# Optimization experiments

Measured on AMD Instinct MI355X. Metric: run time of the kernel, lower is better.

The kernel has to match this reference:

```python
import jax, jax.numpy as jnp
import numpy as np

N_Q = 50000
B, T = 256, 500
DK = 128      # q_embed_dim == memory_key_state_dim == final_fc_dim
DV = 256      # qa_embed_dim == memory_value_state_dim
M = 50        # memory_size

def setup_inputs() -> dict:
    key = jax.random.key(0)
    ks = jax.random.split(key, 12)
    q_data = jax.random.randint(ks[0], (B, T), 0, N_Q + 1)
    qa_data = jax.random.randint(ks[1], (B, T), 0, 2 * N_Q + 1)
    # target in {-1, 0, 1}; -1 = padding (masked out)
    u = jax.random.uniform(ks[2], (B * T, 1))
    target = jnp.floor(u * 3.0) - 1.0
    # embedding tables with padding_idx=0 zeroed
    q_tab = (jax.random.normal(ks[3], (N_Q + 1, DK)) * (2.0 / DK) ** 0.5).at[0].set(0.0)
    qa_tab = (jax.random.normal(ks[4], (2 * N_Q + 1, DV)) * (2.0 / DV) ** 0.5).at[0].set(0.0)
    Mk = jax.random.normal(ks[5], (M, DK)) * (2.0 / DK) ** 0.5
    Mv0 = jax.random.normal(ks[6], (M, DV)) * (2.0 / DV) ** 0.5
    We = jax.random.normal(ks[7], (DV, DV)) * (1.0 / DV) ** 0.5
    be = jnp.zeros((DV,))
    Wa = jax.random.normal(ks[8], (DV, DV)) * (1.0 / DV) ** 0.5
    ba = jnp.zeros((DV,))
    Wr = jax.random.normal(ks[9], (DK, DV + DK)) * (2.0 / (DV + DK)) ** 0.5
    br = jnp.zeros((DK,))
    Wp = jax.random.normal(ks[10], (1, DK)) * (2.0 / DK) ** 0.5
    bp = jnp.zeros((1,))
    return dict(q_data=q_data, qa_data=qa_data, target=target, q_tab=q_tab,
                qa_tab=qa_tab, Mk=Mk, Mv0=Mv0, We=We, be=be, Wa=Wa, ba=ba,
                Wr=Wr, br=br, Wp=Wp, bp=bp)


def reference(q_data, qa_data, target, q_tab, qa_tab, Mk, Mv0, We, be, Wa, ba, Wr, br, Wp, bp):
    b, t = q_data.shape
    q_e = q_tab[q_data]            # (B,T,DK)
    qa_e = qa_tab[qa_data]         # (B,T,DV)
    wr_mask = (q_data >= 1).astype(q_e.dtype)  # write gate per step
    Mv_init = jnp.broadcast_to(Mv0[None], (b, M, DV))

    def step(Mv, xs):
        q, qa, m = xs              # q:(B,DK) qa:(B,DV) m:(B,)
        w = jax.nn.softmax(q @ Mk.T, axis=-1)          # (B,M) correlation weight
        read = jnp.einsum('bm,bmd->bd', w, Mv)         # (B,DV)
        e = jax.nn.sigmoid(qa @ We.T + be)             # erase (B,DV)
        a = jnp.tanh(qa @ Wa.T + ba)                   # add   (B,DV)
        new = Mv * (1.0 - w[:, :, None] * e[:, None, :]) + w[:, :, None] * a[:, None, :]
        Mv = jnp.where(m[:, None, None] > 0, new, Mv)  # only write for non-pad steps
        return Mv, read

    _, reads = jax.lax.scan(step, Mv_init,
                            (q_e.transpose(1, 0, 2), qa_e.transpose(1, 0, 2), wr_mask.T))
    reads = reads.transpose(1, 0, 2)                    # (B,T,DV)
    feat = jnp.concatenate([reads, q_e], axis=2).reshape(b * t, DV + DK)
    h = jnp.tanh(feat @ Wr.T + br)                      # (B*T,DK)
    pred = h @ Wp.T + bp                                # (B*T,1) logits
    mask = target >= 0
    # stable BCE-with-logits per element
    per = jnp.maximum(pred, 0.0) - pred * target + jnp.log1p(jnp.exp(-jnp.abs(pred)))
    n_valid = jnp.maximum(jnp.sum(mask.astype(pred.dtype)), 1.0)
    loss = jnp.sum(jnp.where(mask, per, 0.0)) / n_valid
    probs = jax.nn.sigmoid(pred)
    return loss, probs
```

## Files before the change

kernel.cpp:

```cpp
#include <hip/hip_runtime.h>
#include <hip/hip_bf16.h>
#include <stdint.h>


#define BATCH 256
#define TLEN  500
#define DKQ   128
#define DVV   256
#define MSZ   50
#define NROWS 128000
#define GSZ   10

__device__ __forceinline__ float bfs(uint16_t u){
  union { uint32_t u; float f; } v; v.u = ((uint32_t)u) << 16; return v.f;
}
__device__ __forceinline__ uint16_t f2b(float x){
  union { __hip_bfloat16 h; uint16_t u; } c; c.h = __float2bfloat16(x); return c.u;
}

typedef __attribute__((ext_vector_type(8))) short bf16x8;
typedef __attribute__((ext_vector_type(4))) float f32x4;

__device__ __forceinline__ void gl_lds16(const void* g, void* l){
  __builtin_amdgcn_global_load_lds(
      (const __attribute__((address_space(1))) void*)g,
      (__attribute__((address_space(3))) void*)l, 16, 0, 0);
}

__global__ __launch_bounds__(128, 1) void k_w(
    const int* __restrict__ q_data, const float* __restrict__ q_tab,
    const float* __restrict__ Mk, float* __restrict__ w_ws)
{
  __shared__ float mk[MSZ*DKQ];
  __shared__ float wt[128*52];
  const int tid = threadIdx.x;
  for (int li = tid; li < 1600; li += 128)
    ((float4*)mk)[li] = ((const float4*)Mk)[li];
  __syncthreads();

  const int row = blockIdx.x*128 + tid;
  const int qi = q_data[row];
  const float4* qrow = (const float4*)(q_tab + (size_t)qi*DKQ);

  float acc[MSZ];
  #pragma unroll
  for (int m=0;m<MSZ;m++) acc[m] = 0.f;

  #pragma unroll 1
  for (int c8=0; c8<8; c8++){
    float4 q0 = qrow[c8*4+0], q1 = qrow[c8*4+1], q2 = qrow[c8*4+2], q3 = qrow[c8*4+3];
    #pragma unroll
    for (int m=0;m<MSZ;m++){
      const float4* mr = (const float4*)&mk[m*DKQ + c8*16];
      float4 a = mr[0], b = mr[1], cc = mr[2], d = mr[3];
      float s = acc[m];
      s = fmaf(q0.x,a.x,s);  s = fmaf(q0.y,a.y,s);  s = fmaf(q0.z,a.z,s);  s = fmaf(q0.w,a.w,s);
      s = fmaf(q1.x,b.x,s);  s = fmaf(q1.y,b.y,s);  s = fmaf(q1.z,b.z,s);  s = fmaf(q1.w,b.w,s);
      s = fmaf(q2.x,cc.x,s); s = fmaf(q2.y,cc.y,s); s = fmaf(q2.z,cc.z,s); s = fmaf(q2.w,cc.w,s);
      s = fmaf(q3.x,d.x,s);  s = fmaf(q3.y,d.y,s);  s = fmaf(q3.z,d.z,s);  s = fmaf(q3.w,d.w,s);
      acc[m] = s;
    }
  }
  float mx = acc[0];
  #pragma unroll
  for (int m=1;m<MSZ;m++) mx = fmaxf(mx, acc[m]);
  float s = 0.f;
  #pragma unroll
  for (int m=0;m<MSZ;m++){ acc[m] = __expf(acc[m]-mx); s += acc[m]; }
  float inv = 1.0f / s;
  #pragma unroll
  for (int m=0;m<MSZ;m++) wt[tid*52+m] = acc[m]*inv;
  wt[tid*52+50] = 0.f; wt[tid*52+51] = 0.f;
  __syncthreads();
  float4* dst = (float4*)(w_ws + (size_t)blockIdx.x*128*52);
  const float4* src = (const float4*)wt;
  for (int li = tid; li < 1664; li += 128) dst[li] = src[li];
}

__global__ __launch_bounds__(256) void k_cvt(
    const float* __restrict__ qa_tab, const float* __restrict__ We,
    const float* __restrict__ Wa, uint16_t* __restrict__ qa_bf,
    uint16_t* __restrict__ wcomb)
{
  const size_t n_qa4 = 6400064;
  const size_t n_w4  = 32768;
  size_t stride = (size_t)gridDim.x*blockDim.x;
  for (size_t i = (size_t)blockIdx.x*256 + threadIdx.x; i < n_qa4 + n_w4; i += stride){
    float4 v;
    if (i < n_qa4){
      v = ((const float4*)qa_tab)[i];
      ushort4 o; o.x=f2b(v.x); o.y=f2b(v.y); o.z=f2b(v.z); o.w=f2b(v.w);
      ((ushort4*)qa_bf)[i] = o;
    } else {
      size_t j = i - n_qa4;
      size_t f = j*4;
      int col = (int)(f >> 8), k = (int)(f & 255);
      const float* srcp = (col < 256) ? (We + (size_t)col*256 + k)
                                      : (Wa + (size_t)(col-256)*256 + k);
      v = *(const float4*)srcp;
      ushort4 o; o.x=f2b(v.x); o.y=f2b(v.y); o.z=f2b(v.z); o.w=f2b(v.w);
      ((ushort4*)wcomb)[j] = o;
    }
  }
}

__global__ __launch_bounds__(256) void k_cvt2(
    const float* __restrict__ q_tab, const float* __restrict__ Wr,
    uint16_t* __restrict__ q_bf, uint16_t* __restrict__ wr_bf)
{
  const size_t n_q4  = 1600032;
  const size_t n_wr4 = 12288;
  size_t stride = (size_t)gridDim.x*blockDim.x;
  for (size_t i = (size_t)blockIdx.x*256 + threadIdx.x; i < n_q4 + n_wr4; i += stride){
    if (i < n_q4){
      float4 v = ((const float4*)q_tab)[i];
      ushort4 o; o.x=f2b(v.x); o.y=f2b(v.y); o.z=f2b(v.z); o.w=f2b(v.w);
      ((ushort4*)q_bf)[i] = o;
    } else {
      size_t j = i - n_q4;
      float4 v = ((const float4*)Wr)[j];
      ushort4 o; o.x=f2b(v.x); o.y=f2b(v.y); o.z=f2b(v.z); o.w=f2b(v.w);
      ((ushort4*)wr_bf)[j] = o;
    }
  }
}

__global__ __launch_bounds__(256, 2) void k_ea(
    const int* __restrict__ qa_data, const uint16_t* __restrict__ qa_bf,
    const uint16_t* __restrict__ wcomb, const float* __restrict__ be,
    const float* __restrict__ ba, __hip_bfloat16* __restrict__ ea_ws)
{
  __shared__ uint16_t Ab[128*32];
  __shared__ uint16_t Bb[128*32];
  const int tid = threadIdx.x;
  const int lane = tid & 63, wid = tid >> 6;
  const int braw = blockIdx.x;
  const int nb = (braw >> 3) & 3;
  const int mb = (braw & 7) | ((braw >> 5) << 3);
  const int rb = mb*128, cb = nb*128;

  const char* qac = (const char*)qa_bf;
  size_t aoff0, aoff1;
  {
    int r0 = wid*32 + (lane>>2);
    aoff0 = (size_t)qa_data[rb + r0]*512      + (size_t)(lane&3)*16;
    aoff1 = (size_t)qa_data[rb + r0 + 16]*512 + (size_t)(lane&3)*16;
  }
  const char* wcb = (const char*)wcomb;
  size_t boff0 = (size_t)(cb + wid*32 + (lane>>2))*512 + (size_t)(lane&3)*16;
  size_t boff1 = boff0 + 16*512;

  const int wr = (wid>>1)*64, wc = (wid&1)*64;
  float bias[4];
  #pragma unroll
  for (int tj=0;tj<4;tj++){
    int colg = cb + wc + tj*16 + (lane&15);
    bias[tj] = (nb<2) ? be[colg] : ba[colg-256];
  }

  f32x4 acc[4][4];
  #pragma unroll
  for (int i=0;i<4;i++){
    #pragma unroll
    for (int j=0;j<4;j++) acc[i][j] = (f32x4)(0.f);
  }

  #pragma unroll 1
  for (int kc=0; kc<8; kc++){
    __syncthreads();
    gl_lds16(qac + aoff0 + (size_t)kc*64, &Ab[(wid*2+0)*512]);
    gl_lds16(qac + aoff1 + (size_t)kc*64, &Ab[(wid*2+1)*512]);
    gl_lds16(wcb + boff0 + (size_t)kc*64, &Bb[(wid*2+0)*512]);
    gl_lds16(wcb + boff1 + (size_t)kc*64, &Bb[(wid*2+1)*512]);
    __syncthreads();
    bf16x8 af[4], bfr[4];
    #pragma unroll
    for (int ti=0;ti<4;ti++)
      af[ti] = *(const bf16x8*)&Ab[(wr + ti*16 + (lane&15))*32 + (lane>>4)*8];
    #pragma unroll
    for (int tj=0;tj<4;tj++)
      bfr[tj] = *(const bf16x8*)&Bb[(wc + tj*16 + (lane&15))*32 + (lane>>4)*8];
    #pragma unroll
    for (int ti=0;ti<4;ti++){
      #pragma unroll
      for (int tj=0;tj<4;tj++)
        acc[ti][tj] = __builtin_amdgcn_mfma_f32_16x16x32_bf16(af[ti], bfr[tj], acc[ti][tj], 0, 0, 0);
    }
  }
  const int rq = (lane>>4)*4, cl = lane&15;
  #pragma unroll
  for (int ti=0;ti<4;ti++){
    #pragma unroll
    for (int r=0;r<4;r++){
      int row = rb + wr + ti*16 + rq + r;
      __hip_bfloat16* orow = ea_ws + (size_t)row*512 + cb + wc;
      #pragma unroll
      for (int tj=0;tj<4;tj++){
        float x = acc[ti][tj][r] + bias[tj];
        float v = (nb<2) ? (1.f/(1.f+__expf(-x)))
                         : (1.f - 2.f/(__expf(2.f*x)+1.f));
        orow[tj*16 + cl] = __float2bfloat16(v);
      }
    }
  }
}

__global__ __launch_bounds__(512, 1) void k_scan(
    const int* __restrict__ q_data, const float* __restrict__ w_ws,
    const uint16_t* __restrict__ ea_ws, const float* __restrict__ Mv0,
    __hip_bfloat16* __restrict__ reads_ws)
{
  __shared__ float wbuf[2][GSZ*52];
  __shared__ float part[2][256];
  const int tid = threadIdx.x;
  const int d = tid & 255, h = tid >> 8;
  const int base = blockIdx.x*TLEN;

  float Mv[28];
  #pragma unroll
  for (int qq=0; qq<7; qq++){
    #pragma unroll
    for (int e=0;e<4;e++){
      int quad = 2*qq + h, m = quad*4 + e;
      Mv[qq*4+e] = (quad <= 12 && m < MSZ) ? Mv0[m*256 + d] : 0.f;
    }
  }

  float4 wreg;
  uint16_t ecur[GSZ], acur[GSZ], enxt[GSZ], anxt[GSZ];
  int qcur[GSZ], qnxt[GSZ];

  if (tid < 130) wreg = ((const float4*)(w_ws + (size_t)base*52))[tid];
  #pragma unroll
  for (int j=0;j<GSZ;j++){
    ecur[j] = ea_ws[(size_t)(base+j)*512 + d];
    acur[j] = ea_ws[(size_t)(base+j)*512 + 256 + d];
    qcur[j] = q_data[base+j];
  }
  if (tid < 130) ((float4*)wbuf[0])[tid] = wreg;
  __syncthreads();

  #pragma unroll 1
  for (int g=0; g<50; g++){
    if (g < 49){
      const int sn = base + (g+1)*GSZ;
      if (tid < 130) wreg = ((const float4*)(w_ws + (size_t)sn*52))[tid];
      #pragma unroll
      for (int j=0;j<GSZ;j++){
        enxt[j] = ea_ws[(size_t)(sn+j)*512 + d];
        anxt[j] = ea_ws[(size_t)(sn+j)*512 + 256 + d];
        qnxt[j] = q_data[sn+j];
      }
    }
    const float* wb = wbuf[g&1];
    const int s0 = base + g*GSZ;
    #pragma unroll
    for (int j=0;j<GSZ;j++){
      const float4* wq = (const float4*)(wb + j*52);
      float ef = bfs(ecur[j]), af = bfs(acur[j]);
      float4 wv[7];
      #pragma unroll
      for (int qq=0; qq<6; qq++) wv[qq] = wq[2*qq + h];
      if (h == 0) wv[6] = wq[12];
      float r0=0.f, r1=0.f, r2=0.f, r3=0.f;
      #pragma unroll
      for (int qq=0; qq<6; qq++){
        r0 = fmaf(wv[qq].x, Mv[qq*4+0], r0);
        r1 = fmaf(wv[qq].y, Mv[qq*4+1], r1);
        r2 = fmaf(wv[qq].z, Mv[qq*4+2], r2);
        r3 = fmaf(wv[qq].w, Mv[qq*4+3], r3);
      }
      if (h == 0){
        r0 = fmaf(wv[6].x, Mv[24], r0);
        r1 = fmaf(wv[6].y, Mv[25], r1);
        r2 = fmaf(wv[6].z, Mv[26], r2);
        r3 = fmaf(wv[6].w, Mv[27], r3);
      }
      float rp = (r0+r1)+(r2+r3);
      if (h == 0) part[j&1][d] = rp;
      __syncthreads();
      if (h == 1){
        float rd = rp + part[j&1][d];
        reads_ws[(size_t)(s0+j)*256 + d] = __float2bfloat16(rd);
      }
      if (qcur[j] > 0){
        #pragma unroll
        for (int qq=0; qq<6; qq++){
          { float tt = fmaf(ef, Mv[qq*4+0], -af); Mv[qq*4+0] = fmaf(-wv[qq].x, tt, Mv[qq*4+0]); }
          { float tt = fmaf(ef, Mv[qq*4+1], -af); Mv[qq*4+1] = fmaf(-wv[qq].y, tt, Mv[qq*4+1]); }
          { float tt = fmaf(ef, Mv[qq*4+2], -af); Mv[qq*4+2] = fmaf(-wv[qq].z, tt, Mv[qq*4+2]); }
          { float tt = fmaf(ef, Mv[qq*4+3], -af); Mv[qq*4+3] = fmaf(-wv[qq].w, tt, Mv[qq*4+3]); }
        }
        if (h == 0){
          { float tt = fmaf(ef, Mv[24], -af); Mv[24] = fmaf(-wv[6].x, tt, Mv[24]); }
          { float tt = fmaf(ef, Mv[25], -af); Mv[25] = fmaf(-wv[6].y, tt, Mv[25]); }
        }
      }
    }
    if (g < 49){
      if (tid < 130) ((float4*)wbuf[(g+1)&1])[tid] = wreg;
      #pragma unroll
      for (int j=0;j<GSZ;j++){ ecur[j]=enxt[j]; acur[j]=anxt[j]; qcur[j]=qnxt[j]; }
    }
    __syncthreads();
  }
}

__global__ __launch_bounds__(256, 2) void k_final(
    const int* __restrict__ q_data, const uint16_t* __restrict__ q_bf,
    const uint16_t* __restrict__ reads16, const uint16_t* __restrict__ wr_bf,
    const float* __restrict__ br, const float* __restrict__ Wp,
    const float* __restrict__ bp, const float* __restrict__ target,
    float* __restrict__ out, float* __restrict__ parts)
{
  __shared__ uint16_t Ab[64*32];
  __shared__ uint16_t Bb[128*32];
  __shared__ float redbuf[8];
  const int tid = threadIdx.x;
  const int lane = tid & 63, wid = tid >> 6;
  const int rb = blockIdx.x * 64;

  const char* rdc = (const char*)reads16;
  const char* qbc = (const char*)q_bf;
  const char* wrc = (const char*)wr_bf;
  const int arow = wid*16 + (lane>>2);
  size_t aoff_r = (size_t)(rb+arow)*512 + (size_t)(lane&3)*16;
  size_t aoff_q = (size_t)q_data[rb+arow]*256 + (size_t)(lane&3)*16;
  size_t boff0  = (size_t)(wid*32 + (lane>>2))*768 + (size_t)(lane&3)*16;
  size_t boff1  = boff0 + 16*768;

  f32x4 acc[8];
  #pragma unroll
  for (int tj=0;tj<8;tj++) acc[tj] = (f32x4)(0.f);

  #pragma unroll 1
  for (int kc=0; kc<12; kc++){
    __syncthreads();
    if (kc < 8) gl_lds16(rdc + aoff_r + (size_t)kc*64,     &Ab[wid*512]);
    else        gl_lds16(qbc + aoff_q + (size_t)(kc-8)*64, &Ab[wid*512]);
    gl_lds16(wrc + boff0 + (size_t)kc*64, &Bb[(wid*2+0)*512]);
    gl_lds16(wrc + boff1 + (size_t)kc*64, &Bb[(wid*2+1)*512]);
    __syncthreads();
    bf16x8 af = *(const bf16x8*)&Ab[(wid*16 + (lane&15))*32 + (lane>>4)*8];
    #pragma unroll
    for (int tj=0;tj<8;tj++){
      bf16x8 bf = *(const bf16x8*)&Bb[(tj*16 + (lane&15))*32 + (lane>>4)*8];
      acc[tj] = __builtin_amdgcn_mfma_f32_16x16x32_bf16(af, bf, acc[tj], 0, 0, 0);
    }
  }
  const int cl = lane & 15, rq = lane >> 4;
  float p[4] = {0.f,0.f,0.f,0.f};
  #pragma unroll
  for (int tj=0;tj<8;tj++){
    int cg = tj*16 + cl;
    float brv = br[cg], wpv = Wp[cg];
    #pragma unroll
    for (int r=0;r<4;r++){
      float x = acc[tj][r] + brv;
      float hh = 1.f - 2.f/(__expf(2.f*x)+1.f);
      p[r] = fmaf(hh, wpv, p[r]);
    }
  }
  #pragma unroll
  for (int off=1; off<16; off<<=1){
    #pragma unroll
    for (int r=0;r<4;r++) p[r] += __shfl_xor(p[r], off);
  }
  float bpv = bp[0];
  float lsum = 0.f, csum = 0.f;
  if (cl == 0){
    #pragma unroll
    for (int r=0;r<4;r++){
      int row = rb + wid*16 + rq*4 + r;
      float pred = p[r] + bpv;
      out[1 + row] = 1.f/(1.f + __expf(-pred));
      float tg = target[row];
      if (tg >= 0.f){
        lsum += fmaxf(pred, 0.f) - pred*tg + log1pf(__expf(-fabsf(pred)));
        csum += 1.f;
      }
    }
  }
  #pragma unroll
  for (int off=16; off<64; off<<=1){
    lsum += __shfl_xor(lsum, off);
    csum += __shfl_xor(csum, off);
  }
  if (lane == 0){ redbuf[wid*2] = lsum; redbuf[wid*2+1] = csum; }
  __syncthreads();
  if (tid == 0){
    parts[blockIdx.x]        = redbuf[0]+redbuf[2]+redbuf[4]+redbuf[6];
    parts[2000 + blockIdx.x] = redbuf[1]+redbuf[3]+redbuf[5]+redbuf[7];
  }
}

__global__ __launch_bounds__(256) void k_loss(
    const float* __restrict__ parts, float* __restrict__ out)
{
  __shared__ float red[8];
  const int tid = threadIdx.x;
  float l = 0.f, cn = 0.f;
  for (int i = tid; i < 2000; i += 256){ l += parts[i]; cn += parts[2000+i]; }
  #pragma unroll
  for (int off=32; off>0; off>>=1){ l += __shfl_xor(l, off); cn += __shfl_xor(cn, off); }
  if ((tid & 63) == 0){ red[(tid>>6)*2] = l; red[(tid>>6)*2+1] = cn; }
  __syncthreads();
  if (tid == 0){
    float L = red[0]+red[2]+red[4]+red[6];
    float C = red[1]+red[3]+red[5]+red[7];
    out[0] = L / fmaxf(C, 1.f);
  }
}

extern "C" void kernel_launch(void* const* d_in, const int* in_sizes, int n_in,
                              void* d_out, int out_size, void* d_ws, size_t ws_size,
                              hipStream_t stream) {
  const int*   q_data  = (const int*)d_in[0];
  const int*   qa_data = (const int*)d_in[1];
  const float* target  = (const float*)d_in[2];
  const float* q_tab   = (const float*)d_in[3];
  const float* qa_tab  = (const float*)d_in[4];
  const float* Mk  = (const float*)d_in[5];
  const float* Mv0 = (const float*)d_in[6];
  const float* We  = (const float*)d_in[7];
  const float* be  = (const float*)d_in[8];
  const float* Wa  = (const float*)d_in[9];
  const float* ba  = (const float*)d_in[10];
  const float* Wr  = (const float*)d_in[11];
  const float* br  = (const float*)d_in[12];
  const float* Wp  = (const float*)d_in[13];
  const float* bp  = (const float*)d_in[14];

  char* ws = (char*)d_ws;
  float*          w_ws     = (float*)ws;
  __hip_bfloat16* ea_ws    = (__hip_bfloat16*)(ws + 26624000);
  uint16_t*       qa_bf    = (uint16_t*)(ws + 157696000);
  uint16_t*       wcomb    = (uint16_t*)(ws + 208896512);
  __hip_bfloat16* reads_ws = (__hip_bfloat16*)(ws + 157696000);
  float*          parts    = (float*)ws;
  uint16_t*       q_bf     = (uint16_t*)(ws + 2000000);
  uint16_t*       wr_bf    = (uint16_t*)(ws + 16000000);

  float* out = (float*)d_out;

  k_w    <<<1000, 128, 0, stream>>>(q_data, q_tab, Mk, w_ws);
  k_cvt  <<<2048, 256, 0, stream>>>(qa_tab, We, Wa, qa_bf, wcomb);
  k_ea   <<<4000, 256, 0, stream>>>(qa_data, qa_bf, wcomb, be, ba, ea_ws);
  k_scan <<<256,  512, 0, stream>>>(q_data, w_ws, (const uint16_t*)ea_ws, Mv0, reads_ws);
  k_cvt2 <<<1024, 256, 0, stream>>>(q_tab, Wr, q_bf, wr_bf);
  k_final<<<2000, 256, 0, stream>>>(q_data, q_bf, (const uint16_t*)reads_ws, wr_bf, br, Wp, bp, target, out, parts);
  k_loss <<<1,    256, 0, stream>>>(parts, out);
}
```

Baseline: 653.0 us.

## Interleave erase/add outputs, pair scan threads via shuffle, enlarge final GEMM tile

k_ea now writes erase and add values interleaved per column, so k_scan fetches both with a single 32-bit load. k_scan maps the two memory halves to adjacent lanes and combines partial reads with a lane shuffle, which removes the per-step __syncthreads and LDS exchange. It also replaces the h==0 branches with a mask multiply and raises launch bounds to 2 blocks per SM. k_final processes 128 rows per block with two A tiles to get more reuse of the B tile, halving the grid and the partial-sum count.

```diff
diff --git a/kernel.cpp b/kernel.cpp
--- a/kernel.cpp
+++ b/kernel.cpp
@@ -13,6 +13,12 @@
 
 __device__ __forceinline__ float bfs(uint16_t u){
   union { uint32_t u; float f; } v; v.u = ((uint32_t)u) << 16; return v.f;
+}
+__device__ __forceinline__ float bflo32(uint32_t u){
+  union { uint32_t u; float f; } v; v.u = u << 16; return v.f;
+}
+__device__ __forceinline__ float bfhi32(uint32_t u){
+  union { uint32_t u; float f; } v; v.u = u & 0xffff0000u; return v.f;
 }
 __device__ __forceinline__ uint16_t f2b(float x){
   union { __hip_bfloat16 h; uint16_t u; } c; c.h = __float2bfloat16(x); return c.u;
@@ -128,7 +134,7 @@
 __global__ __launch_bounds__(256, 2) void k_ea(
     const int* __restrict__ qa_data, const uint16_t* __restrict__ qa_bf,
     const uint16_t* __restrict__ wcomb, const float* __restrict__ be,
-    const float* __restrict__ ba, __hip_bfloat16* __restrict__ ea_ws)
+    const float* __restrict__ ba, uint16_t* __restrict__ ea16)
 {
   __shared__ uint16_t Ab[128*32];
   __shared__ uint16_t Bb[128*32];
@@ -188,53 +194,55 @@
     }
   }
   const int rq = (lane>>4)*4, cl = lane&15;
+  const int isa = (nb >= 2);
+  const int cbase = (cb & 255) + wc;
   #pragma unroll
   for (int ti=0;ti<4;ti++){
     #pragma unroll
     for (int r=0;r<4;r++){
       int row = rb + wr + ti*16 + rq + r;
-      __hip_bfloat16* orow = ea_ws + (size_t)row*512 + cb + wc;
+      uint16_t* orow = ea16 + (size_t)row*512;
       #pragma unroll
       for (int tj=0;tj<4;tj++){
         float x = acc[ti][tj][r] + bias[tj];
         float v = (nb<2) ? (1.f/(1.f+__expf(-x)))
                          : (1.f - 2.f/(__expf(2.f*x)+1.f));
-        orow[tj*16 + cl] = __float2bfloat16(v);
-      }
-    }
-  }
-}
-
-__global__ __launch_bounds__(512, 1) void k_scan(
+        orow[2*(cbase + tj*16 + cl) + isa] = f2b(v);
+      }
+    }
+  }
+}
+
+__global__ __launch_bounds__(512, 2) void k_scan(
     const int* __restrict__ q_data, const float* __restrict__ w_ws,
-    const uint16_t* __restrict__ ea_ws, const float* __restrict__ Mv0,
+    const uint32_t* __restrict__ ea32, const float* __restrict__ Mv0,
     __hip_bfloat16* __restrict__ reads_ws)
 {
   __shared__ float wbuf[2][GSZ*52];
-  __shared__ float part[2][256];
   const int tid = threadIdx.x;
-  const int d = tid & 255, h = tid >> 8;
+  const int d = tid >> 1, h = tid & 1;
   const int base = blockIdx.x*TLEN;
+  const float hm = (h == 0) ? 1.f : 0.f;
 
   float Mv[28];
   #pragma unroll
   for (int qq=0; qq<7; qq++){
+    int quad = 2*qq + h;
     #pragma unroll
     for (int e=0;e<4;e++){
-      int quad = 2*qq + h, m = quad*4 + e;
-      Mv[qq*4+e] = (quad <= 12 && m < MSZ) ? Mv0[m*256 + d] : 0.f;
+      int m = quad*4 + e;
+      Mv[qq*4+e] = (m < MSZ) ? Mv0[m*256 + d] : 0.f;
     }
   }
 
   float4 wreg;
-  uint16_t ecur[GSZ], acur[GSZ], enxt[GSZ], anxt[GSZ];
+  uint32_t eacur[GSZ], eanxt[GSZ];
   int qcur[GSZ], qnxt[GSZ];
 
   if (tid < 130) wreg = ((const float4*)(w_ws + (size_t)base*52))[tid];
   #pragma unroll
   for (int j=0;j<GSZ;j++){
-    ecur[j] = ea_ws[(size_t)(base+j)*512 + d];
-    acur[j] = ea_ws[(size_t)(base+j)*512 + 256 + d];
+    eacur[j] = ea32[(size_t)(base+j)*256 + d];
     qcur[j] = q_data[base+j];
   }
   if (tid < 130) ((float4*)wbuf[0])[tid] = wreg;
@@ -247,8 +255,7 @@
       if (tid < 130) wreg = ((const float4*)(w_ws + (size_t)sn*52))[tid];
       #pragma unroll
       for (int j=0;j<GSZ;j++){
-        enxt[j] = ea_ws[(size_t)(sn+j)*512 + d];
-        anxt[j] = ea_ws[(size_t)(sn+j)*512 + 256 + d];
+        eanxt[j] = ea32[(size_t)(sn+j)*256 + d];
         qnxt[j] = q_data[sn+j];
       }
     }
@@ -257,50 +264,36 @@
     #pragma unroll
     for (int j=0;j<GSZ;j++){
       const float4* wq = (const float4*)(wb + j*52);
-      float ef = bfs(ecur[j]), af = bfs(acur[j]);
+      float ef = bflo32(eacur[j]), af = bfhi32(eacur[j]);
       float4 wv[7];
       #pragma unroll
       for (int qq=0; qq<6; qq++) wv[qq] = wq[2*qq + h];
-      if (h == 0) wv[6] = wq[12];
+      { float4 t = wq[12]; wv[6] = make_float4(t.x*hm, t.y*hm, t.z*hm, t.w*hm); }
       float r0=0.f, r1=0.f, r2=0.f, r3=0.f;
       #pragma unroll
-      for (int qq=0; qq<6; qq++){
+      for (int qq=0; qq<7; qq++){
         r0 = fmaf(wv[qq].x, Mv[qq*4+0], r0);
         r1 = fmaf(wv[qq].y, Mv[qq*4+1], r1);
         r2 = fmaf(wv[qq].z, Mv[qq*4+2], r2);
         r3 = fmaf(wv[qq].w, Mv[qq*4+3], r3);
       }
-      if (h == 0){
-        r0 = fmaf(wv[6].x, Mv[24], r0);
-        r1 = fmaf(wv[6].y, Mv[25], r1);
-        r2 = fmaf(wv[6].z, Mv[26], r2);
-        r3 = fmaf(wv[6].w, Mv[27], r3);
-      }
       float rp = (r0+r1)+(r2+r3);
-      if (h == 0) part[j&1][d] = rp;
-      __syncthreads();
-      if (h == 1){
-        float rd = rp + part[j&1][d];
-        reads_ws[(size_t)(s0+j)*256 + d] = __float2bfloat16(rd);
-      }
+      float rd = rp + __shfl_xor(rp, 1);
+      if (h == 0) reads_ws[(size_t)(s0+j)*256 + d] = __float2bfloat16(rd);
       if (qcur[j] > 0){
         #pragma unroll
-        for (int qq=0; qq<6; qq++){
+        for (int qq=0; qq<7; qq++){
           { float tt = fmaf(ef, Mv[qq*4+0], -af); Mv[qq*4+0] = fmaf(-wv[qq].x, tt, Mv[qq*4+0]); }
           { float tt = fmaf(ef, Mv[qq*4+1], -af); Mv[qq*4+1] = fmaf(-wv[qq].y, tt, Mv[qq*4+1]); }
           { float tt = fmaf(ef, Mv[qq*4+2], -af); Mv[qq*4+2] = fmaf(-wv[qq].z, tt, Mv[qq*4+2]); }
           { float tt = fmaf(ef, Mv[qq*4+3], -af); Mv[qq*4+3] = fmaf(-wv[qq].w, tt, Mv[qq*4+3]); }
         }
-        if (h == 0){
-          { float tt = fmaf(ef, Mv[24], -af); Mv[24] = fmaf(-wv[6].x, tt, Mv[24]); }
-          { float tt = fmaf(ef, Mv[25], -af); Mv[25] = fmaf(-wv[6].y, tt, Mv[25]); }
-        }
       }
     }
     if (g < 49){
       if (tid < 130) ((float4*)wbuf[(g+1)&1])[tid] = wreg;
       #pragma unroll
-      for (int j=0;j<GSZ;j++){ ecur[j]=enxt[j]; acur[j]=anxt[j]; qcur[j]=qnxt[j]; }
+      for (int j=0;j<GSZ;j++){ eacur[j]=eanxt[j]; qcur[j]=qnxt[j]; }
     }
     __syncthreads();
   }
@@ -313,71 +306,95 @@
     const float* __restrict__ bp, const float* __restrict__ target,
     float* __restrict__ out, float* __restrict__ parts)
 {
-  __shared__ uint16_t Ab[64*32];
+  __shared__ uint16_t Ab[128*32];
   __shared__ uint16_t Bb[128*32];
   __shared__ float redbuf[8];
   const int tid = threadIdx.x;
   const int lane = tid & 63, wid = tid >> 6;
-  const int rb = blockIdx.x * 64;
+  const int rb = blockIdx.x * 128;
 
   const char* rdc = (const char*)reads16;
   const char* qbc = (const char*)q_bf;
   const char* wrc = (const char*)wr_bf;
-  const int arow = wid*16 + (lane>>2);
-  size_t aoff_r = (size_t)(rb+arow)*512 + (size_t)(lane&3)*16;
-  size_t aoff_q = (size_t)q_data[rb+arow]*256 + (size_t)(lane&3)*16;
+  const int ar0 = wid*32 + (lane>>2), ar1 = ar0 + 16;
+  size_t aoffr0 = (size_t)(rb+ar0)*512 + (size_t)(lane&3)*16;
+  size_t aoffr1 = (size_t)(rb+ar1)*512 + (size_t)(lane&3)*16;
+  size_t aoffq0 = (size_t)q_data[rb+ar0]*256 + (size_t)(lane&3)*16;
+  size_t aoffq1 = (size_t)q_data[rb+ar1]*256 + (size_t)(lane&3)*16;
   size_t boff0  = (size_t)(wid*32 + (lane>>2))*768 + (size_t)(lane&3)*16;
   size_t boff1  = boff0 + 16*768;
 
-  f32x4 acc[8];
-  #pragma unroll
-  for (int tj=0;tj<8;tj++) acc[tj] = (f32x4)(0.f);
+  f32x4 acc[2][8];
+  #pragma unroll
+  for (int ti=0;ti<2;ti++){
+    #pragma unroll
+    for (int tj=0;tj<8;tj++) acc[ti][tj] = (f32x4)(0.f);
+  }
 
   #pragma unroll 1
   for (int kc=0; kc<12; kc++){
     __syncthreads();
-    if (kc < 8) gl_lds16(rdc + aoff_r + (size_t)kc*64,     &Ab[wid*512]);
-    else        gl_lds16(qbc + aoff_q + (size_t)(kc-8)*64, &Ab[wid*512]);
+    if (kc < 8){
+      gl_lds16(rdc + aoffr0 + (size_t)kc*64, &Ab[(wid*2+0)*512]);
+      gl_lds16(rdc + aoffr1 + (size_t)kc*64, &Ab[(wid*2+1)*512]);
+    } else {
+      gl_lds16(qbc + aoffq0 + (size_t)(kc-8)*64, &Ab[(wid*2+0)*512]);
+      gl_lds16(qbc + aoffq1 + (size_t)(kc-8)*64, &Ab[(wid*2+1)*512]);
+    }
     gl_lds16(wrc + boff0 + (size_t)kc*64, &Bb[(wid*2+0)*512]);
     gl_lds16(wrc + boff1 + (size_t)kc*64, &Bb[(wid*2+1)*512]);
     __syncthreads();
-    bf16x8 af = *(const bf16x8*)&Ab[(wid*16 + (lane&15))*32 + (lane>>4)*8];
+    bf16x8 af[2];
+    #pragma unroll
+    for (int ti=0;ti<2;ti++)
+      af[ti] = *(const bf16x8*)&Ab[(wid*32 + ti*16 + (lane&15))*32 + (lane>>4)*8];
     #pragma unroll
     for (int tj=0;tj<8;tj++){
       bf16x8 bf = *(const bf16x8*)&Bb[(tj*16 + (lane&15))*32 + (lane>>4)*8];
-      acc[tj] = __builtin_amdgcn_mfma_f32_16x16x32_bf16(af, bf, acc[tj], 0, 0, 0);
+      #pragma unroll
+      for (int ti=0;ti<2;ti++)
+        acc[ti][tj] = __builtin_amdgcn_mfma_f32_16x16x32_bf16(af[ti], bf, acc[ti][tj], 0, 0, 0);
     }
   }
   const int cl = lane & 15, rq = lane >> 4;
-  float p[4] = {0.f,0.f,0.f,0.f};
+  float p[2][4] = {{0.f,0.f,0.f,0.f},{0.f,0.f,0.f,0.f}};
   #pragma unroll
   for (int tj=0;tj<8;tj++){
     int cg = tj*16 + cl;
     float brv = br[cg], wpv = Wp[cg];
     #pragma unroll
-    for (int r=0;r<4;r++){
-      float x = acc[tj][r] + brv;
-      float hh = 1.f - 2.f/(__expf(2.f*x)+1.f);
-      p[r] = fmaf(hh, wpv, p[r]);
+    for (int ti=0;ti<2;ti++){
+      #pragma unroll
+      for (int r=0;r<4;r++){
+        float x = acc[ti][tj][r] + brv;
+        float hh = 1.f - 2.f/(__expf(2.f*x)+1.f);
+        p[ti][r] = fmaf(hh, wpv, p[ti][r]);
+      }
     }
   }
   #pragma unroll
   for (int off=1; off<16; off<<=1){
     #pragma unroll
-    for (int r=0;r<4;r++) p[r] += __shfl_xor(p[r], off);
+    for (int ti=0;ti<2;ti++){
+      #pragma unroll
+      for (int r=0;r<4;r++) p[ti][r] += __shfl_xor(p[ti][r], off);
+    }
   }
   float bpv = bp[0];
   float lsum = 0.f, csum = 0.f;
   if (cl == 0){
     #pragma unroll
-    for (int r=0;r<4;r++){
-      int row = rb + wid*16 + rq*4 + r;
-      float pred = p[r] + bpv;
-      out[1 + row] = 1.f/(1.f + __expf(-pred));
-      float tg = target[row];
-      if (tg >= 0.f){
-        lsum += fmaxf(pred, 0.f) - pred*tg + log1pf(__expf(-fabsf(pred)));
-        csum += 1.f;
+    for (int ti=0;ti<2;ti++){
+      #pragma unroll
+      for (int r=0;r<4;r++){
+        int row = rb + wid*32 + ti*16 + rq*4 + r;
+        float pred = p[ti][r] + bpv;
+        out[1 + row] = 1.f/(1.f + __expf(-pred));
+        float tg = target[row];
+        if (tg >= 0.f){
+          lsum += fmaxf(pred, 0.f) - pred*tg + log1pf(__expf(-fabsf(pred)));
+          csum += 1.f;
+        }
       }
     }
   }
@@ -390,7 +407,7 @@
   __syncthreads();
   if (tid == 0){
     parts[blockIdx.x]        = redbuf[0]+redbuf[2]+redbuf[4]+redbuf[6];
-    parts[2000 + blockIdx.x] = redbuf[1]+redbuf[3]+redbuf[5]+redbuf[7];
+    parts[1000 + blockIdx.x] = redbuf[1]+redbuf[3]+redbuf[5]+redbuf[7];
   }
 }
 
@@ -400,7 +417,7 @@
   __shared__ float red[8];
   const int tid = threadIdx.x;
   float l = 0.f, cn = 0.f;
-  for (int i = tid; i < 2000; i += 256){ l += parts[i]; cn += parts[2000+i]; }
+  for (int i = tid; i < 1000; i += 256){ l += parts[i]; cn += parts[1000+i]; }
   #pragma unroll
   for (int off=32; off>0; off>>=1){ l += __shfl_xor(l, off); cn += __shfl_xor(cn, off); }
   if ((tid & 63) == 0){ red[(tid>>6)*2] = l; red[(tid>>6)*2+1] = cn; }
@@ -433,7 +450,7 @@
 
   char* ws = (char*)d_ws;
   float*          w_ws     = (float*)ws;
-  __hip_bfloat16* ea_ws    = (__hip_bfloat16*)(ws + 26624000);
+  uint16_t*       ea16     = (uint16_t*)(ws + 26624000);
   uint16_t*       qa_bf    = (uint16_t*)(ws + 157696000);
   uint16_t*       wcomb    = (uint16_t*)(ws + 208896512);
   __hip_bfloat16* reads_ws = (__hip_bfloat16*)(ws + 157696000);
@@ -445,9 +462,9 @@
 
   k_w    <<<1000, 128, 0, stream>>>(q_data, q_tab, Mk, w_ws);
   k_cvt  <<<2048, 256, 0, stream>>>(qa_tab, We, Wa, qa_bf, wcomb);
-  k_ea   <<<4000, 256, 0, stream>>>(qa_data, qa_bf, wcomb, be, ba, ea_ws);
-  k_scan <<<256,  512, 0, stream>>>(q_data, w_ws, (const uint16_t*)ea_ws, Mv0, reads_ws);
+  k_ea   <<<4000, 256, 0, stream>>>(qa_data, qa_bf, wcomb, be, ba, ea16);
+  k_scan <<<256,  512, 0, stream>>>(q_data, w_ws, (const uint32_t*)ea16, Mv0, reads_ws);
   k_cvt2 <<<1024, 256, 0, stream>>>(q_tab, Wr, q_bf, wr_bf);
-  k_final<<<2000, 256, 0, stream>>>(q_data, q_bf, (const uint16_t*)reads_ws, wr_bf, br, Wp, bp, target, out, parts);
+  k_final<<<1000, 256, 0, stream>>>(q_data, q_bf, (const uint16_t*)reads_ws, wr_bf, br, Wp, bp, target, out, parts);
   k_loss <<<1,    256, 0, stream>>>(parts, out);
 }
```

Result: slower. 671.8 us (+2.9%).
